# Kernel optimization log

Measured on AMD Instinct MI355X. Metric: run time of the kernel, lower is better.

The kernel has to match this reference:

```python
import jax, jax.numpy as jnp
import numpy as np

PS = 8; STRIDE = 1; NVALS = 31
DELTA = 0.05; ETA = 0.01; TAU = 0.1
B = 2; CIN = 32; H = 64; W = 64
HP = (H - PS) // STRIDE + 1
WP = (W - PS) // STRIDE + 1
TWO_PI = 2.0 * np.pi

# patch-local coordinate grid (torch.meshgrid 'ij': y varies along rows)
_lin = np.linspace(-1.0, 1.0, PS).astype(np.float32)
YG = jnp.asarray(np.tile(_lin[:, None], (1, PS)))[None, :, :, None, None]  # [1,ps,ps,1,1]
XG = jnp.asarray(np.tile(_lin[None, :], (PS, 1)))[None, :, :, None, None]

ANGLE_RANGE = jnp.asarray(np.linspace(0.0, TWO_PI, NVALS + 1, dtype=np.float32)[:NVALS])
XY_RANGE = jnp.asarray(np.linspace(-3.0, 3.0, NVALS, dtype=np.float32))

# unfold/fold index maps: pixel (hp*stride + px, wp*stride + py)
RI = jnp.arange(PS)[:, None] + STRIDE * jnp.arange(HP)[None, :]  # [ps,hp]
CI = jnp.arange(PS)[:, None] + STRIDE * jnp.arange(WP)[None, :]  # [ps,wp]
R4 = RI[:, None, :, None]  # [ps,1,hp,1]
C4 = CI[None, :, None, :]  # [1,ps,1,wp]


def conv1x1(x, w):
    return jnp.einsum('bchw,oc->bohw', x, w)


def bn(x, gamma, beta, eps=1e-5):
    # BatchNorm2d in training mode: batch statistics, biased variance
    m = x.mean(axis=(0, 2, 3), keepdims=True)
    v = x.var(axis=(0, 2, 3), keepdims=True)
    return gamma[None, :, None, None] * (x - m) * jax.lax.rsqrt(v + eps) + beta[None, :, None, None]


def silu(x):
    return x * jax.nn.sigmoid(x)


def params_to_distances(params):
    # params: [n,5,hp,wp] -> dists [n,2,ps,ps,hp,wp]
    x0 = params[:, 3][:, None, None]  # [n,1,1,hp,wp]
    y0 = params[:, 4][:, None, None]
    ang = jnp.sort(jnp.mod(params[:, :3], TWO_PI), axis=1)
    a1 = ang[:, 0][:, None, None]
    a2 = ang[:, 1][:, None, None]
    a3 = ang[:, 2][:, None, None]
    a4 = 0.5 * (a1 + a3) + jnp.where(jnp.mod(0.5 * (a1 - a3), TWO_PI) >= np.pi, np.pi, 0.0)

    def g(dt):
        return (dt / np.pi - 1.0) ** 35

    def line(a):
        return -jnp.sin(a) * (XG - x0) + jnp.cos(a) * (YG - y0)

    d42 = jnp.mod(a2 - a4, TWO_PI)
    sgn42 = jnp.where(d42 < np.pi, 1.0, -1.0)
    dist42 = sgn42 * jnp.minimum(sgn42 * line(a4), -sgn42 * line(a2)) + g(d42) * TAU
    d13 = jnp.mod(a3 - a1, TWO_PI)
    sgn13 = jnp.where(d13 < np.pi, 1.0, -1.0)
    dist13 = sgn13 * jnp.minimum(sgn13 * line(a1), -sgn13 * line(a3)) + g(d13) * TAU
    return jnp.stack([dist13, dist42], axis=1)


def wedges_of(dists):
    hd = 0.5 * (1.0 + (2.0 / np.pi) * jnp.arctan(dists / ETA))
    h0, h1 = hd[:, 0], hd[:, 1]
    return jnp.stack([1.0 - h0, h0 * (1.0 - h1), h0 * h1], axis=1)  # [n,3,ps,ps,hp,wp]


def dcp(params, imgp):
    # params [n,5,hp,wp], imgp [c,ps,ps,hp,wp]
    dists = params_to_distances(params)
    w = wedges_of(dists)
    wsum = w.sum(axis=(2, 3))  # [n,3,hp,wp]
    cnum = jnp.einsum('cxyHW,nkxyHW->nckHW', imgp, w)
    colors = cnum / (wsum[:, None] + 1e-10)  # [n,c,3,hp,wp]
    patches = jnp.einsum('nkxyHW,nckHW->ncxyHW', w, colors)
    return dists, colors, patches


def boundaries_of(dists):
    d1, d2 = dists[:, 0:1], dists[:, 1:2]
    mad = jnp.where(d1 < 0.0, -d1,
                    jnp.where(d2 < 0.0, jnp.minimum(d1, -d2), jnp.minimum(d1, d2)))
    return 1.0 / (1.0 + (mad / DELTA) ** 2)


def fold(patches):
    # [B,C,ps,ps,hp,wp] -> [B,C,H,W] (sum over overlapping patches)
    Bn, C = patches.shape[:2]
    return jnp.zeros((Bn, C, H, W), patches.dtype).at[:, :, R4, C4].add(patches)


def forward(x, reduce_w, reduce_gamma, reduce_beta, fb_w, fb_gamma, fb_beta, fi_w, fi_gamma, fi_beta):
    xr = silu(bn(conv1x1(x, reduce_w), reduce_gamma, reduce_beta))  # [B,3,H,W]
    imgp = xr[:, :, R4, C4]  # unfold -> [B,3,ps,ps,hp,wp]
    num_patches = jnp.zeros((H, W), xr.dtype).at[R4, C4].add(
        jnp.ones((PS, PS, HP, WP), xr.dtype))

    params = jnp.zeros((x.shape[0], 5, HP, WP), xr.dtype)

    def make_step(i, prange):
        def step(p_b, imgp_b):
            pq = jnp.repeat(p_b[None], NVALS, axis=0)  # [n,5,hp,wp]
            pq = pq.at[:, i].add(prange[:, None, None])
            _, _, patches = dcp(pq, imgp_b)
            loss = ((imgp_b[None] - patches) ** 2).mean(axis=(2, 3)).sum(axis=1)  # [n,hp,wp]
            best = jnp.argmin(loss, axis=0)
            vals = jnp.take_along_axis(pq[:, i], best[None], axis=0)[0]
            return p_b.at[i].set(vals)
        return step

    for i in range(5):  # coordinate descent over 3 angles then x0, y0
        prange = ANGLE_RANGE if i < 3 else XY_RANGE
        params = jax.vmap(make_step(i, prange))(params, imgp)

    def finalize(p_b, imgp_b):
        dists, _, patches = dcp(p_b[None], imgp_b)
        return patches[0], boundaries_of(dists)[0]

    patches_all, lb_all = jax.vmap(finalize)(params, imgp)
    smoothed = fold(patches_all) / num_patches[None, None]  # [B,3,H,W]
    gb = fold(lb_all) / num_patches[None, None]             # [B,1,H,W]
    gb3 = jnp.broadcast_to(gb, (gb.shape[0], 3, H, W))
    boundaries = silu(bn(conv1x1(gb3, fb_w), fb_gamma, fb_beta))
    image = silu(bn(conv1x1(smoothed, fi_w), fi_gamma, fi_beta))
    return boundaries, image


def setup_inputs() -> dict:
    key = jax.random.key(0)
    ks = jax.random.split(key, 4)
    return {
        'x': jax.random.normal(ks[0], (B, CIN, H, W), jnp.float32),
        'reduce_w': jax.random.normal(ks[1], (3, CIN), jnp.float32) * 0.1,
        'reduce_gamma': jnp.ones((3,), jnp.float32),
        'reduce_beta': jnp.zeros((3,), jnp.float32),
        'fb_w': jax.random.normal(ks[2], (1, 3), jnp.float32) * 0.3,
        'fb_gamma': jnp.ones((1,), jnp.float32),
        'fb_beta': jnp.zeros((1,), jnp.float32),
        'fi_w': jax.random.normal(ks[3], (1, 3), jnp.float32) * 0.3,
        'fi_gamma': jnp.ones((1,), jnp.float32),
        'fi_beta': jnp.zeros((1,), jnp.float32),
    }


def reference(x, reduce_w, reduce_gamma, reduce_beta, fb_w, fb_gamma, fb_beta, fi_w, fi_gamma, fi_beta):
    return forward(x, reduce_w, reduce_gamma, reduce_beta, fb_w, fb_gamma, fb_beta, fi_w, fi_gamma, fi_beta)
```

## Files before the change

### kernel.cpp

```cpp
#include <hip/hip_runtime.h>
#include <math.h>

#define B_    2
#define CIN_  32
#define H_    64
#define W_    64
#define HP_   57
#define WP_   57
#define NP_   (B_*HP_*WP_)
#define NVALS_ 31

#define XR_OFF   0
#define FP_OFF   24576
#define FG_OFF   49152
#define ST_OFF   57344
#define WS_TOTAL 57360

static __device__ __forceinline__ float mod2pi(float x) {
    const float TP = (float)(2.0 * M_PI);
    float m = fmodf(x, TP);
    return (m < 0.0f) ? (m + TP) : m;
}
static __device__ __forceinline__ float pow35f(float t) {
    float t2 = t * t, t4 = t2 * t2, t8 = t4 * t4, t16 = t8 * t8, t32 = t16 * t16;
    return t32 * t2 * t;
}
static __device__ __forceinline__ float siluf(float x) {
    return x / (1.0f + expf(-x));
}
static __device__ __forceinline__ float wave_sum(float v) {
#pragma unroll
    for (int m = 1; m < 64; m <<= 1) v += __shfl_xor(v, m);
    return v;
}
static __device__ __forceinline__ float lin_of(int k) {
    return (float)(-1.0 + (double)k * (2.0 / 7.0));
}

struct Geo {
    float X1, Y1, X3, Y3;
    float X4, Y4, X2, Y2;
    float sgn13, sgn42, g13, g42, x0, y0;
};

static __device__ void setup_geo(float p0, float p1, float p2, float p3, float p4,
                                 Geo& G) {
    const float PIF = (float)M_PI;
    float m0 = mod2pi(p0), m1 = mod2pi(p1), m2 = mod2pi(p2);
    float lo = fminf(m0, m1), hi = fmaxf(m0, m1);
    float a1 = fminf(lo, m2);
    float a3 = fmaxf(hi, m2);
    float a2 = fmaxf(fminf(hi, m2), lo);
    float hm = mod2pi(0.5f * (a1 - a3));
    float a4 = 0.5f * (a1 + a3) + ((hm >= PIF) ? PIF : 0.0f);
    float d42 = mod2pi(a2 - a4);
    G.sgn42 = (d42 < PIF) ? 1.0f : -1.0f;
    G.g42 = pow35f(d42 / PIF - 1.0f) * 0.1f;
    float d13 = mod2pi(a3 - a1);
    G.sgn13 = (d13 < PIF) ? 1.0f : -1.0f;
    G.g13 = pow35f(d13 / PIF - 1.0f) * 0.1f;
    float s1 = sinf(a1), c1 = cosf(a1);
    float s2 = sinf(a2), c2 = cosf(a2);
    float s3 = sinf(a3), c3 = cosf(a3);
    float s4 = sinf(a4), c4 = cosf(a4);
    G.X1 = -G.sgn13 * s1;  G.Y1 =  G.sgn13 * c1;
    G.X3 =  G.sgn13 * s3;  G.Y3 = -G.sgn13 * c3;
    G.X4 = -G.sgn42 * s4;  G.Y4 =  G.sgn42 * c4;
    G.X2 =  G.sgn42 * s2;  G.Y2 = -G.sgn42 * c2;
    G.x0 = p3; G.y0 = p4;
}

static __device__ __forceinline__ void dists_at(const Geo& G, float xg, float yg,
                                                float& d13, float& d42) {
    float dx = xg - G.x0, dy = yg - G.y0;
    float u1 = G.X1 * dx + G.Y1 * dy;
    float u3 = G.X3 * dx + G.Y3 * dy;
    float u4 = G.X4 * dx + G.Y4 * dy;
    float u2 = G.X2 * dx + G.Y2 * dy;
    d13 = G.sgn13 * fminf(u1, u3) + G.g13;
    d42 = G.sgn42 * fminf(u4, u2) + G.g42;
}

static __device__ __forceinline__ void wedge_of(float d13, float d42,
                                                float& w0, float& w1, float& w2) {
    const float C2OPI = (float)(2.0 / M_PI);
    float hd0 = 0.5f * (1.0f + C2OPI * atanf(d13 * 100.0f));
    float hd1 = 0.5f * (1.0f + C2OPI * atanf(d42 * 100.0f));
    w0 = 1.0f - hd0;
    w1 = hd0 * (1.0f - hd1);
    w2 = hd0 * hd1;
}

__global__ __launch_bounds__(128) void head_in_conv(const float* __restrict__ x,
                                                    const float* __restrict__ rw,
                                                    float* __restrict__ xr,
                                                    float* __restrict__ st,
                                                    float4* __restrict__ foldZ) {
    const int e = blockIdx.x * 128 + threadIdx.x;
    foldZ[e] = make_float4(0.0f, 0.0f, 0.0f, 0.0f);
    const int b = e >> 12, rem = e & 4095;
    const float* xp = x + (size_t)b * CIN_ * 4096 + rem;
    float a0 = 0.0f, a1 = 0.0f, a2 = 0.0f;
#pragma unroll
    for (int c = 0; c < CIN_; ++c) {
        float xv = xp[c * 4096];
        a0 += rw[c] * xv;
        a1 += rw[32 + c] * xv;
        a2 += rw[64 + c] * xv;
    }
    xr[(b * 3 + 0) * 4096 + rem] = a0;
    xr[(b * 3 + 1) * 4096 + rem] = a1;
    xr[(b * 3 + 2) * 4096 + rem] = a2;
    float s0 = wave_sum(a0), q0 = wave_sum(a0 * a0);
    float s1 = wave_sum(a1), q1 = wave_sum(a1 * a1);
    float s2 = wave_sum(a2), q2 = wave_sum(a2 * a2);
    if ((threadIdx.x & 63) == 0) {
        atomicAdd(&st[0], s0); atomicAdd(&st[1], s1); atomicAdd(&st[2], s2);
        atomicAdd(&st[3], q0); atomicAdd(&st[4], q1); atomicAdd(&st[5], q2);
    }
}

__global__ __launch_bounds__(256) void mega_kernel(const float* __restrict__ xr,
                                                   const float* __restrict__ gamma,
                                                   const float* __restrict__ beta,
                                                   const float* __restrict__ st,
                                                   float* __restrict__ foldP,
                                                   float* __restrict__ foldG) {
    __shared__ float s_img[4][192];
    __shared__ float s_lin[8];
    const int t = threadIdx.x;
    if (t < 8) s_lin[t] = lin_of(t);
    const int lg = t >> 6, lane = t & 63;
    const int patch = blockIdx.x * 4 + lg;
    const bool active = (patch < NP_);
    int b = 0, hp = 0, wp = 0;
    if (active) {
        b = patch / (HP_ * WP_);
        int pi = patch - b * (HP_ * WP_);
        hp = pi / WP_; wp = pi - hp * WP_;
        const int pr = lane >> 3, pc = lane & 7;
        const int goff = ((hp + pr) << 6) + (wp + pc);
#pragma unroll
        for (int c = 0; c < 3; ++c) {
            float mean = st[c] / 8192.0f;
            float var  = st[3 + c] / 8192.0f - mean * mean;
            float sc = gamma[c] / sqrtf(var + 1e-5f);
            float sh = beta[c] - mean * sc;
            float v  = xr[((b * 3 + c) << 12) + goff];
            s_img[lg][64 * c + lane] = siluf(v * sc + sh);
        }
    }
    __syncthreads();
    if (!active) return;

    const int cand = lane >> 1;
    const int half = lane & 1;
    const float* img = s_img[lg] + half * 32;
    const int yoff = half << 2;

    float is0 = 0, is1 = 0, is2 = 0;
#pragma unroll
    for (int i = 0; i < 32; ++i) {
        is0 += img[i]; is1 += img[64 + i]; is2 += img[128 + i];
    }
    is0 += __shfl_xor(is0, 1); is1 += __shfl_xor(is1, 1); is2 += __shfl_xor(is2, 1);

    float p0 = 0.0f, p1 = 0.0f, p2 = 0.0f, p3 = 0.0f, p4 = 0.0f;

#pragma unroll 1
    for (int step = 0; step < 5; ++step) {
        const float base = (step == 0) ? p0 : (step == 1) ? p1 :
                           (step == 2) ? p2 : (step == 3) ? p3 : p4;
        const int ci = (cand < NVALS_) ? cand : (NVALS_ - 1);
        float add;
        if (step < 3) add = (float)((double)ci * (6.283185307179586476925286766559 / 31.0));
        else          add = (float)(-3.0 + (double)ci * 0.2);
        const float pv = base + add;
        Geo G;
        setup_geo((step == 0) ? pv : p0, (step == 1) ? pv : p1,
                  (step == 2) ? pv : p2, (step == 3) ? pv : p3,
                  (step == 4) ? pv : p4, G);

        float ws0 = 0, ws1 = 0;
        float cn00 = 0, cn01 = 0, cn10 = 0, cn11 = 0, cn20 = 0, cn21 = 0;
        float g00 = 0, g01 = 0, g11 = 0;
#pragma unroll 1
        for (int r = 0; r < 4; ++r) {
            const float yg = s_lin[yoff + r];
            const float dy = yg - G.y0;
            const float t1 = G.Y1 * dy, t3 = G.Y3 * dy;
            const float t4 = G.Y4 * dy, t2 = G.Y2 * dy;
#pragma unroll
            for (int cth = 0; cth < 8; ++cth) {
                const int i = r * 8 + cth;
                const float dx = s_lin[cth] - G.x0;
                float u1 = G.X1 * dx + t1;
                float u3 = G.X3 * dx + t3;
                float u4 = G.X4 * dx + t4;
                float u2 = G.X2 * dx + t2;
                float d13 = G.sgn13 * fminf(u1, u3) + G.g13;
                float d42 = G.sgn42 * fminf(u4, u2) + G.g42;
                float w0, w1, w2;
                wedge_of(d13, d42, w0, w1, w2);
                float i0 = img[i], i1 = img[64 + i], i2 = img[128 + i];
                ws0 += w0; ws1 += w1;
                cn00 += i0 * w0; cn01 += i0 * w1;
                cn10 += i1 * w0; cn11 += i1 * w1;
                cn20 += i2 * w0; cn21 += i2 * w1;
                g00 += w0 * w0; g01 += w0 * w1; g11 += w1 * w1;
            }
        }
        ws0 += __shfl_xor(ws0, 1); ws1 += __shfl_xor(ws1, 1);
        cn00 += __shfl_xor(cn00, 1); cn01 += __shfl_xor(cn01, 1);
        cn10 += __shfl_xor(cn10, 1); cn11 += __shfl_xor(cn11, 1);
        cn20 += __shfl_xor(cn20, 1); cn21 += __shfl_xor(cn21, 1);
        g00 += __shfl_xor(g00, 1); g01 += __shfl_xor(g01, 1); g11 += __shfl_xor(g11, 1);

        float ws2  = 64.0f - ws0 - ws1;
        float cn02 = is0 - cn00 - cn01;
        float cn12 = is1 - cn10 - cn11;
        float cn22 = is2 - cn20 - cn21;
        float g02  = ws0 - g00 - g01;
        float g12  = ws1 - g01 - g11;
        float g22  = ws2 - g02 - g12;

        float r0 = 1.0f / (ws0 + 1e-10f);
        float r1 = 1.0f / (ws1 + 1e-10f);
        float r2 = 1.0f / (ws2 + 1e-10f);
        float c00 = cn00 * r0, c01 = cn01 * r1, c02 = cn02 * r2;
        float c10 = cn10 * r0, c11 = cn11 * r1, c12 = cn12 * r2;
        float c20 = cn20 * r0, c21 = cn21 * r1, c22 = cn22 * r2;

        float loss =
            (c00 * c00 * g00 + c01 * c01 * g11 + c02 * c02 * g22
             + 2.0f * (c00 * c01 * g01 + c00 * c02 * g02 + c01 * c02 * g12)
             - 2.0f * (c00 * cn00 + c01 * cn01 + c02 * cn02))
          + (c10 * c10 * g00 + c11 * c11 * g11 + c12 * c12 * g22
             + 2.0f * (c10 * c11 * g01 + c10 * c12 * g02 + c11 * c12 * g12)
             - 2.0f * (c10 * cn10 + c11 * cn11 + c12 * cn12))
          + (c20 * c20 * g00 + c21 * c21 * g11 + c22 * c22 * g22
             + 2.0f * (c20 * c21 * g01 + c20 * c22 * g02 + c21 * c22 * g12)
             - 2.0f * (c20 * cn20 + c21 * cn21 + c22 * cn22));
        if (cand >= NVALS_) loss = INFINITY;

        float bl = loss; int bi = cand;
#pragma unroll
        for (int off = 32; off > 0; off >>= 1) {
            float ol = __shfl_down(bl, (unsigned)off);
            int   oi = __shfl_down(bi, (unsigned)off);
            if (ol < bl || (ol == bl && oi < bi)) { bl = ol; bi = oi; }
        }
        bi = __shfl(bi, 0);
        float badd;
        if (step < 3) badd = (float)((double)bi * (6.283185307179586476925286766559 / 31.0));
        else          badd = (float)(-3.0 + (double)bi * 0.2);
        const float bv = base + badd;
        if (step == 0) p0 = bv; else if (step == 1) p1 = bv;
        else if (step == 2) p2 = bv; else if (step == 3) p3 = bv; else p4 = bv;
    }

    {
        Geo G; setup_geo(p0, p1, p2, p3, p4, G);
        const int pr = lane >> 3, pc = lane & 7;
        float xg = s_lin[pc], yg = s_lin[pr];
        float d13, d42;
        dists_at(G, xg, yg, d13, d42);
        float w0, w1, w2;
        wedge_of(d13, d42, w0, w1, w2);
        float i0 = s_img[lg][lane];
        float i1 = s_img[lg][64 + lane];
        float i2 = s_img[lg][128 + lane];

        float r[12] = { w0, w1, w2,
                        i0 * w0, i0 * w1, i0 * w2,
                        i1 * w0, i1 * w1, i1 * w2,
                        i2 * w0, i2 * w1, i2 * w2 };
#pragma unroll
        for (int m = 1; m < 64; m <<= 1) {
#pragma unroll
            for (int j = 0; j < 12; ++j) r[j] += __shfl_xor(r[j], m);
        }
        float col[3][3];
#pragma unroll
        for (int c = 0; c < 3; ++c) {
            col[c][0] = r[3 + c * 3 + 0] / (r[0] + 1e-10f);
            col[c][1] = r[3 + c * 3 + 1] / (r[1] + 1e-10f);
            col[c][2] = r[3 + c * 3 + 2] / (r[2] + 1e-10f);
        }
        float o0 = w0 * col[0][0] + w1 * col[0][1] + w2 * col[0][2];
        float o1 = w0 * col[1][0] + w1 * col[1][1] + w2 * col[1][2];
        float o2 = w0 * col[2][0] + w1 * col[2][1] + w2 * col[2][2];

        float mad = (d13 < 0.0f) ? -d13 : ((d42 < 0.0f) ? fminf(d13, -d42) : fminf(d13, d42));
        float tt = mad / 0.05f;
        float lb = 1.0f / (1.0f + tt * tt);

        const int off = ((hp + pr) << 6) + (wp + pc);
        atomicAdd(&foldP[(b * 3 + 0) * 4096 + off], o0);
        atomicAdd(&foldP[(b * 3 + 1) * 4096 + off], o1);
        atomicAdd(&foldP[(b * 3 + 2) * 4096 + off], o2);
        atomicAdd(&foldG[b * 4096 + off], lb);
    }
}

static __device__ __forceinline__ float np_count(int tpos) {
    int lo = (tpos - 56 > 0) ? (tpos - 56) : 0;
    int hi = (tpos < 7) ? tpos : 7;
    return (float)(hi - lo + 1);
}

__global__ __launch_bounds__(1024) void head_out(const float* __restrict__ foldP,
                                                 const float* __restrict__ foldG,
                                                 const float* __restrict__ fb_w,
                                                 const float* __restrict__ fb_g,
                                                 const float* __restrict__ fb_b,
                                                 const float* __restrict__ fi_w,
                                                 const float* __restrict__ fi_g,
                                                 const float* __restrict__ fi_b,
                                                 float* __restrict__ out) {
    __shared__ float sB[8192];
    __shared__ float sI[8192];
    __shared__ float red[16][4];
    __shared__ float s_sc[4];
    const int t = threadIdx.x;
    float sb = 0, qb = 0, si = 0, qi = 0;
#pragma unroll
    for (int k = 0; k < 8; ++k) {
        const int e = t + 1024 * k;
        const int b = e >> 12, h = (e >> 6) & 63, w = e & 63;
        const float inv = 1.0f / (np_count(h) * np_count(w));
        float gv = foldG[e] * inv;
        float vb = fb_w[0] * gv + fb_w[1] * gv + fb_w[2] * gv;
        const int off = (h << 6) + w;
        float v0 = foldP[(b * 3 + 0) * 4096 + off] * inv;
        float v1 = foldP[(b * 3 + 1) * 4096 + off] * inv;
        float v2 = foldP[(b * 3 + 2) * 4096 + off] * inv;
        float vi = fi_w[0] * v0 + fi_w[1] * v1 + fi_w[2] * v2;
        sB[e] = vb; sI[e] = vi;
        sb += vb; qb += vb * vb; si += vi; qi += vi * vi;
    }
    sb = wave_sum(sb); qb = wave_sum(qb); si = wave_sum(si); qi = wave_sum(qi);
    const int wid = t >> 6;
    if ((t & 63) == 0) { red[wid][0] = sb; red[wid][1] = qb; red[wid][2] = si; red[wid][3] = qi; }
    __syncthreads();
    if (t == 0) {
        float S = 0, Q = 0, S2 = 0, Q2 = 0;
#pragma unroll
        for (int w = 0; w < 16; ++w) { S += red[w][0]; Q += red[w][1]; S2 += red[w][2]; Q2 += red[w][3]; }
        float meanB = S / 8192.0f,  varB = Q / 8192.0f - meanB * meanB;
        float meanI = S2 / 8192.0f, varI = Q2 / 8192.0f - meanI * meanI;
        float scB = fb_g[0] / sqrtf(varB + 1e-5f);
        float scI = fi_g[0] / sqrtf(varI + 1e-5f);
        s_sc[0] = scB; s_sc[1] = fb_b[0] - meanB * scB;
        s_sc[2] = scI; s_sc[3] = fi_b[0] - meanI * scI;
    }
    __syncthreads();
    const float scB = s_sc[0], shB = s_sc[1], scI = s_sc[2], shI = s_sc[3];
#pragma unroll
    for (int k = 0; k < 8; ++k) {
        const int e = t + 1024 * k;
        out[e]        = siluf(sB[e] * scB + shB);
        out[8192 + e] = siluf(sI[e] * scI + shI);
    }
}

extern "C" void kernel_launch(void* const* d_in, const int* in_sizes, int n_in,
                              void* d_out, int out_size, void* d_ws, size_t ws_size,
                              hipStream_t stream) {
    (void)in_sizes; (void)n_in; (void)out_size; (void)ws_size;
    const float* x        = (const float*)d_in[0];
    const float* reduce_w = (const float*)d_in[1];
    const float* reduce_g = (const float*)d_in[2];
    const float* reduce_b = (const float*)d_in[3];
    const float* fb_w     = (const float*)d_in[4];
    const float* fb_g     = (const float*)d_in[5];
    const float* fb_b     = (const float*)d_in[6];
    const float* fi_w     = (const float*)d_in[7];
    const float* fi_g     = (const float*)d_in[8];
    const float* fi_b     = (const float*)d_in[9];
    float* ws     = (float*)d_ws;
    float* xr     = ws + XR_OFF;
    float* foldP  = ws + FP_OFF;
    float* foldG  = ws + FG_OFF;
    float* st     = ws + ST_OFF;
    float* out    = (float*)d_out;

    hipMemsetAsync(st, 0, 16 * sizeof(float), stream);

    head_in_conv<<<64, 128, 0, stream>>>(x, reduce_w, xr, st, (float4*)foldP);
    mega_kernel<<<(NP_ + 3) / 4, 256, 0, stream>>>(xr, reduce_g, reduce_b, st,
                                                   foldP, foldG);
    head_out<<<1, 1024, 0, stream>>>(foldP, foldG, fb_w, fb_g, fb_b,
                                     fi_w, fi_g, fi_b, out);
}
```

Before: 235.6 us.

## Prescale wedge distances, replace BN stat atomics with per-wave partials, drop memset

The wedge-distance coefficients and the g offsets are pre-multiplied by 100, so the per-pixel atanf argument no longer needs a multiply, and the tt scaling is adjusted to match. The head kernel now writes per-wave partial sums to distinct slots instead of using atomics. Every mega_kernel wave reduces the 128 partials itself, which removes the hipMemsetAsync launch. The patch x-offsets are also hoisted into registers. The cost is redundant stat reduction in each block, and distances are now kept in scaled units.

```diff
diff --git a/kernel.cpp b/kernel.cpp
--- a/kernel.cpp
+++ b/kernel.cpp
@@ -14,7 +14,7 @@
 #define FP_OFF   24576
 #define FG_OFF   49152
 #define ST_OFF   57344
-#define WS_TOTAL 57360
+#define WS_TOTAL 58112
 
 static __device__ __forceinline__ float mod2pi(float x) {
     const float TP = (float)(2.0 * M_PI);
@@ -46,6 +46,7 @@
 static __device__ void setup_geo(float p0, float p1, float p2, float p3, float p4,
                                  Geo& G) {
     const float PIF = (float)M_PI;
+    const float SC = 100.0f;
     float m0 = mod2pi(p0), m1 = mod2pi(p1), m2 = mod2pi(p2);
     float lo = fminf(m0, m1), hi = fmaxf(m0, m1);
     float a1 = fminf(lo, m2);
@@ -55,18 +56,18 @@
     float a4 = 0.5f * (a1 + a3) + ((hm >= PIF) ? PIF : 0.0f);
     float d42 = mod2pi(a2 - a4);
     G.sgn42 = (d42 < PIF) ? 1.0f : -1.0f;
-    G.g42 = pow35f(d42 / PIF - 1.0f) * 0.1f;
+    G.g42 = pow35f(d42 / PIF - 1.0f) * 10.0f;
     float d13 = mod2pi(a3 - a1);
     G.sgn13 = (d13 < PIF) ? 1.0f : -1.0f;
-    G.g13 = pow35f(d13 / PIF - 1.0f) * 0.1f;
+    G.g13 = pow35f(d13 / PIF - 1.0f) * 10.0f;
     float s1 = sinf(a1), c1 = cosf(a1);
     float s2 = sinf(a2), c2 = cosf(a2);
     float s3 = sinf(a3), c3 = cosf(a3);
     float s4 = sinf(a4), c4 = cosf(a4);
-    G.X1 = -G.sgn13 * s1;  G.Y1 =  G.sgn13 * c1;
-    G.X3 =  G.sgn13 * s3;  G.Y3 = -G.sgn13 * c3;
-    G.X4 = -G.sgn42 * s4;  G.Y4 =  G.sgn42 * c4;
-    G.X2 =  G.sgn42 * s2;  G.Y2 = -G.sgn42 * c2;
+    G.X1 = -G.sgn13 * s1 * SC;  G.Y1 =  G.sgn13 * c1 * SC;
+    G.X3 =  G.sgn13 * s3 * SC;  G.Y3 = -G.sgn13 * c3 * SC;
+    G.X4 = -G.sgn42 * s4 * SC;  G.Y4 =  G.sgn42 * c4 * SC;
+    G.X2 =  G.sgn42 * s2 * SC;  G.Y2 = -G.sgn42 * c2 * SC;
     G.x0 = p3; G.y0 = p4;
 }
 
@@ -81,11 +82,11 @@
     d42 = G.sgn42 * fminf(u4, u2) + G.g42;
 }
 
-static __device__ __forceinline__ void wedge_of(float d13, float d42,
+static __device__ __forceinline__ void wedge_of(float d13s, float d42s,
                                                 float& w0, float& w1, float& w2) {
     const float C2OPI = (float)(2.0 / M_PI);
-    float hd0 = 0.5f * (1.0f + C2OPI * atanf(d13 * 100.0f));
-    float hd1 = 0.5f * (1.0f + C2OPI * atanf(d42 * 100.0f));
+    float hd0 = 0.5f * (1.0f + C2OPI * atanf(d13s));
+    float hd1 = 0.5f * (1.0f + C2OPI * atanf(d42s));
     w0 = 1.0f - hd0;
     w1 = hd0 * (1.0f - hd1);
     w2 = hd0 * hd1;
@@ -115,8 +116,10 @@
     float s1 = wave_sum(a1), q1 = wave_sum(a1 * a1);
     float s2 = wave_sum(a2), q2 = wave_sum(a2 * a2);
     if ((threadIdx.x & 63) == 0) {
-        atomicAdd(&st[0], s0); atomicAdd(&st[1], s1); atomicAdd(&st[2], s2);
-        atomicAdd(&st[3], q0); atomicAdd(&st[4], q1); atomicAdd(&st[5], q2);
+        const int wv = (blockIdx.x << 1) | (threadIdx.x >> 6);
+        float* dst = st + wv * 6;
+        dst[0] = s0; dst[1] = s1; dst[2] = s2;
+        dst[3] = q0; dst[4] = q1; dst[5] = q2;
     }
 }
 
@@ -133,6 +136,19 @@
     const int lg = t >> 6, lane = t & 63;
     const int patch = blockIdx.x * 4 + lg;
     const bool active = (patch < NP_);
+
+    float s0, s1, s2, q0, q1, q2;
+    {
+        const float* pa = st + lane * 6;
+        const float* pb = st + (lane + 64) * 6;
+        s0 = wave_sum(pa[0] + pb[0]);
+        s1 = wave_sum(pa[1] + pb[1]);
+        s2 = wave_sum(pa[2] + pb[2]);
+        q0 = wave_sum(pa[3] + pb[3]);
+        q1 = wave_sum(pa[4] + pb[4]);
+        q2 = wave_sum(pa[5] + pb[5]);
+    }
+
     int b = 0, hp = 0, wp = 0;
     if (active) {
         b = patch / (HP_ * WP_);
@@ -140,15 +156,15 @@
         hp = pi / WP_; wp = pi - hp * WP_;
         const int pr = lane >> 3, pc = lane & 7;
         const int goff = ((hp + pr) << 6) + (wp + pc);
-#pragma unroll
-        for (int c = 0; c < 3; ++c) {
-            float mean = st[c] / 8192.0f;
-            float var  = st[3 + c] / 8192.0f - mean * mean;
-            float sc = gamma[c] / sqrtf(var + 1e-5f);
-            float sh = beta[c] - mean * sc;
-            float v  = xr[((b * 3 + c) << 12) + goff];
-            s_img[lg][64 * c + lane] = siluf(v * sc + sh);
-        }
+        float mean0 = s0 / 8192.0f, var0 = q0 / 8192.0f - mean0 * mean0;
+        float mean1 = s1 / 8192.0f, var1 = q1 / 8192.0f - mean1 * mean1;
+        float mean2 = s2 / 8192.0f, var2 = q2 / 8192.0f - mean2 * mean2;
+        float sc0 = gamma[0] / sqrtf(var0 + 1e-5f), sh0 = beta[0] - mean0 * sc0;
+        float sc1 = gamma[1] / sqrtf(var1 + 1e-5f), sh1 = beta[1] - mean1 * sc1;
+        float sc2 = gamma[2] / sqrtf(var2 + 1e-5f), sh2 = beta[2] - mean2 * sc2;
+        s_img[lg][lane]       = siluf(xr[((b * 3 + 0) << 12) + goff] * sc0 + sh0);
+        s_img[lg][64 + lane]  = siluf(xr[((b * 3 + 1) << 12) + goff] * sc1 + sh1);
+        s_img[lg][128 + lane] = siluf(xr[((b * 3 + 2) << 12) + goff] * sc2 + sh2);
     }
     __syncthreads();
     if (!active) return;
@@ -181,6 +197,10 @@
                   (step == 2) ? pv : p2, (step == 3) ? pv : p3,
                   (step == 4) ? pv : p4, G);
 
+        float dxv[8];
+#pragma unroll
+        for (int k = 0; k < 8; ++k) dxv[k] = s_lin[k] - G.x0;
+
         float ws0 = 0, ws1 = 0;
         float cn00 = 0, cn01 = 0, cn10 = 0, cn11 = 0, cn20 = 0, cn21 = 0;
         float g00 = 0, g01 = 0, g11 = 0;
@@ -193,7 +213,7 @@
 #pragma unroll
             for (int cth = 0; cth < 8; ++cth) {
                 const int i = r * 8 + cth;
-                const float dx = s_lin[cth] - G.x0;
+                const float dx = dxv[cth];
                 float u1 = G.X1 * dx + t1;
                 float u3 = G.X3 * dx + t3;
                 float u4 = G.X4 * dx + t4;
@@ -292,7 +312,7 @@
         float o2 = w0 * col[2][0] + w1 * col[2][1] + w2 * col[2][2];
 
         float mad = (d13 < 0.0f) ? -d13 : ((d42 < 0.0f) ? fminf(d13, -d42) : fminf(d13, d42));
-        float tt = mad / 0.05f;
+        float tt = mad * 0.2f;
         float lb = 1.0f / (1.0f + tt * tt);
 
         const int off = ((hp + pr) << 6) + (wp + pc);
@@ -385,8 +405,6 @@
     float* st     = ws + ST_OFF;
     float* out    = (float*)d_out;
 
-    hipMemsetAsync(st, 0, 16 * sizeof(float), stream);
-
     head_in_conv<<<64, 128, 0, stream>>>(x, reduce_w, xr, st, (float4*)foldP);
     mega_kernel<<<(NP_ + 3) / 4, 256, 0, stream>>>(xr, reduce_g, reduce_b, st,
                                                    foldP, foldG);
```

Measured after the change: 236.4 us. Within noise of the previous version (+0.3%).
